# Optimization experiments

Hardware: AMD Instinct MI355X
Metric: run time of the kernel (lower is better)

The kernel has to match this reference:

```python
import jax, jax.numpy as jnp
import numpy as np
from jax import lax


def setup_inputs() -> dict:
    key = jax.random.key(0)
    k1, k2, k3 = jax.random.split(key, 3)
    B, L, T = 1024, 512, 64
    logits = jax.random.normal(k1, (B, L, T), dtype=jnp.float32)
    tags = jax.random.randint(k2, (B, L), 0, T, dtype=jnp.int64)
    mask = jnp.ones((B, L), dtype=jnp.int32)
    trans_m = jax.random.normal(k3, (T, T), dtype=jnp.float32)
    return {"logits": logits, "tags": tags, "mask": mask, "trans_m": trans_m}


def _normalizer(logits_t, mask_t, trans):
    # logits_t: [L, B, T], mask_t: [L, B] float, trans: [T, T]
    alpha0 = logits_t[0]  # [B, T]

    def step(alpha, xs):
        emit, m = xs  # emit [B, T], m [B]
        # alpha[b, i] + trans[i, j] + emit[b, j] -> logsumexp over i
        tmp = alpha[:, :, None] + emit[:, None, :] + trans[None, :, :]  # [B, T, T]
        new_alpha = jax.nn.logsumexp(tmp, axis=1)  # [B, T]
        alpha = jnp.where(m[:, None] > 0, new_alpha, alpha)
        return alpha, None

    alpha, _ = lax.scan(step, alpha0, (logits_t[1:], mask_t[1:]))
    return jax.nn.logsumexp(alpha, axis=1)  # [B]


def _gold_score(logits_t, tags_t, mask_t, trans):
    # logits_t: [L, B, T], tags_t: [L, B] int, mask_t: [L, B] float
    # transition score between consecutive gold tags, masked where next pos is pad
    trans_score = trans[tags_t[:-1], tags_t[1:]] * mask_t[1:]  # [L-1, B]
    # emission score at gold tags, masked at pad positions
    emit = jnp.take_along_axis(logits_t, tags_t[:, :, None], axis=2)[:, :, 0] * mask_t  # [L, B]
    score = (trans_score + emit[:-1]).sum(axis=0) + emit[-1] * mask_t[-1]  # [B]
    return score


def reference(logits, tags, mask, trans_m):
    # forward: feats [B, L, T] -> transpose to [L, B, T]; loss = logZ - gold_score
    logits_t = jnp.transpose(logits, (1, 0, 2)).astype(jnp.float32)  # [L, B, T]
    tags_t = jnp.transpose(tags, (1, 0))  # [L, B]
    mask_t = jnp.transpose(mask, (1, 0)).astype(logits.dtype)  # [L, B]
    all_path = _normalizer(logits_t, mask_t, trans_m)
    gold = _gold_score(logits_t, tags_t, mask_t, trans_m)
    return all_path - gold  # [B] per-sample negative log-likelihood
```

## Files before the change

kernel.cpp:

```cpp
#include <hip/hip_runtime.h>
#include <math.h>


#define TDIM 64
typedef _Float16 f16;
typedef _Float16 f16x2 __attribute__((ext_vector_type(2)));
typedef _Float16 f16x8 __attribute__((ext_vector_type(8)));
typedef float    f32x4 __attribute__((ext_vector_type(4)));

union B8 { f16x8 v; f16x2 p[4]; };

#define MFMA16(A, B, C) __builtin_amdgcn_mfma_f32_16x16x32_f16((A), (B), (C), 0, 0, 0)

__device__ __forceinline__ f16x2 pk2(float a, float b) {
    f16x2 r; r[0] = (f16)a; r[1] = (f16)b; return r;
}

template <int DIR>
__device__ __forceinline__ void run_chain(
    const float* __restrict__ lp,
    const int*   __restrict__ mrow,
    const float* __restrict__ trans,
    int L, int ml, int gl, bool masked,
    float a[16], int& kacc)
{
    f16x8 Af[4][2];
    #pragma unroll
    for (int c = 0; c < 4; ++c) {
        const int mlog = 32*(c>>1) + 8*(ml>>2) + 4*(c&1) + (ml&3);
        #pragma unroll
        for (int kc = 0; kc < 2; ++kc) {
            B8 t;
            #pragma unroll
            for (int e = 0; e < 8; e += 2) {
                const int k0 = 32*kc + 8*gl + e;
                float x0, x1;
                if (DIR == 0) { x0 = trans[k0*TDIM + mlog];  x1 = trans[(k0+1)*TDIM + mlog]; }
                else          { x0 = trans[mlog*TDIM + k0];  x1 = trans[mlog*TDIM + k0 + 1]; }
                t.p[e>>1] = pk2(__expf(x0), __expf(x1));
            }
            Af[c][kc] = t.v;
        }
    }

    #pragma unroll
    for (int i = 0; i < 16; ++i) a[i] = 1.f;
    kacc = 0;

    const int dstep = (DIR == 0) ? TDIM : -TDIM;
    const float* pp = lp + (size_t)((DIR == 0) ? 0 : (L - 1)) * TDIM + 8 * gl;

    float4 Rf[4][4];
    #pragma unroll
    for (int u = 0; u < 4; ++u) {
        Rf[u][0] = *(const float4*)(pp + 0);
        Rf[u][1] = *(const float4*)(pp + 4);
        Rf[u][2] = *(const float4*)(pp + 32);
        Rf[u][3] = *(const float4*)(pp + 36);
        pp += dstep;
    }
    __builtin_amdgcn_sched_barrier(0);

    float Xc[16];
    #pragma unroll
    for (int c = 0; c < 4; ++c) {
        Xc[c*4+0] = __expf(Rf[0][c].x); Xc[c*4+1] = __expf(Rf[0][c].y);
        Xc[c*4+2] = __expf(Rf[0][c].z); Xc[c*4+3] = __expf(Rf[0][c].w);
    }

    const int NS = L >> 1;
    for (int kb = 0; kb < NS/4; ++kb) {
        #pragma unroll
        for (int u = 0; u < 4; ++u) {
            const int st = 4*kb + u;

            Rf[u][0] = *(const float4*)(pp + 0);
            Rf[u][1] = *(const float4*)(pp + 4);
            Rf[u][2] = *(const float4*)(pp + 32);
            Rf[u][3] = *(const float4*)(pp + 36);
            pp += dstep;
            __builtin_amdgcn_sched_barrier(0);

            float cand[16];
            if (DIR == 0 && st == 0) {
                #pragma unroll
                for (int i = 0; i < 16; ++i) cand[i] = Xc[i];
            } else {
                float bsrc[16];
                #pragma unroll
                for (int i = 0; i < 16; ++i) bsrc[i] = (DIR == 0) ? a[i] : a[i]*Xc[i];
                B8 b0, b1;
                #pragma unroll
                for (int h = 0; h < 4; ++h) {
                    b0.p[h] = pk2(bsrc[2*h],     bsrc[2*h+1]);
                    b1.p[h] = pk2(bsrc[8 + 2*h], bsrc[8 + 2*h+1]);
                }
                f32x4 D0 = {0.f,0.f,0.f,0.f}, D1 = {0.f,0.f,0.f,0.f};
                f32x4 D2 = {0.f,0.f,0.f,0.f}, D3 = {0.f,0.f,0.f,0.f};
                D0 = MFMA16(Af[0][0], b0.v, D0); D0 = MFMA16(Af[0][1], b1.v, D0);
                D1 = MFMA16(Af[1][0], b0.v, D1); D1 = MFMA16(Af[1][1], b1.v, D1);
                D2 = MFMA16(Af[2][0], b0.v, D2); D2 = MFMA16(Af[2][1], b1.v, D2);
                D3 = MFMA16(Af[3][0], b0.v, D3); D3 = MFMA16(Af[3][1], b1.v, D3);
                if (DIR == 0) {
                    #pragma unroll
                    for (int r = 0; r < 4; ++r) {
                        cand[r]      = D0[r] * Xc[r];
                        cand[4 + r]  = D1[r] * Xc[4 + r];
                        cand[8 + r]  = D2[r] * Xc[8 + r];
                        cand[12 + r] = D3[r] * Xc[12 + r];
                    }
                } else {
                    #pragma unroll
                    for (int r = 0; r < 4; ++r) {
                        cand[r] = D0[r]; cand[4+r] = D1[r];
                        cand[8+r] = D2[r]; cand[12+r] = D3[r];
                    }
                }
                if (masked) {
                    const int t = (DIR == 0) ? st : (L - 1 - st);
                    const int m = mrow[t];
                    #pragma unroll
                    for (int i = 0; i < 16; ++i) cand[i] = (m > 0) ? cand[i] : a[i];
                }
            }

            const int un = (u + 1) & 3;
            float Xn[16];
            #pragma unroll
            for (int c = 0; c < 4; ++c) {
                Xn[c*4+0] = __expf(Rf[un][c].x); Xn[c*4+1] = __expf(Rf[un][c].y);
                Xn[c*4+2] = __expf(Rf[un][c].z); Xn[c*4+3] = __expf(Rf[un][c].w);
            }

            {
                const float ref = __shfl(cand[0], ml);
                const int eb = (__float_as_int(ref) >> 23) & 255;
                kacc += eb - 117;
                const float s = __int_as_float((unsigned)(244 - eb) << 23);
                #pragma unroll
                for (int i = 0; i < 16; ++i) a[i] = cand[i] * s;
            }
            #pragma unroll
            for (int i = 0; i < 16; ++i) Xc[i] = Xn[i];
        }
    }
}

__global__ __launch_bounds__(256, 1) void crf_mfma_kernel(
    const float* __restrict__ logits,
    const int*   __restrict__ tags,
    const int*   __restrict__ mask,
    const float* __restrict__ trans,
    float* __restrict__ out,
    int L)
{
    const int tid = threadIdx.x;
    const int w   = tid >> 6;
    const int l   = tid & 63;
    const int ml  = l & 15;
    const int gl  = l >> 4;
    const int bg  = blockIdx.x * 16;
    const int bi  = bg + ml;

    __shared__ __align__(16) float zfin[64][16];
    __shared__ float gpart2[2][16];
    __shared__ int   kbuf[16];

    float a[16];
    int   kacc = 0;

    if (w >= 2) {
        const int t0 = (w - 2) * (L >> 1);
        const int*   tb  = tags + (size_t)bi * L;
        const int*   mb  = mask + (size_t)bi * L;
        const float* lbg = logits + (size_t)bi * L * TDIM;
        float gs = 0.f;
        #pragma unroll 4
        for (int i = 0; i < (L >> 3); ++i) {
            const int t  = t0 + gl + 4*i;
            const int tg = tb[t];
            const float mk = (float)mb[t];
            const float em = lbg[(size_t)t * TDIM + tg];
            const float tr = (t > 0) ? trans[tb[t-1] * TDIM + tg] : 0.f;
            gs += mk * (em + tr);
        }
        gs += __shfl_xor(gs, 16);
        gs += __shfl_xor(gs, 32);
        if (l < 16) gpart2[w - 2][l] = gs;
    } else {
        const float* lp   = logits + (size_t)bi * L * TDIM;
        const int*   mrow = mask + (size_t)bi * L;
        const int t0 = (w == 0) ? 0 : (L >> 1);
        bool ok = true;
        {
            const int4* m4 = (const int4*)(mrow + t0);
            #pragma unroll 4
            for (int i = 0; i < 16; ++i) {
                const int4 v = m4[gl * 16 + i];
                ok = ok && (v.x > 0) && (v.y > 0) && (v.z > 0) && (v.w > 0);
            }
        }
        const bool masked = !__all(ok ? 1 : 0);
        if (w == 0) run_chain<0>(lp, mrow, trans, L, ml, gl, masked, a, kacc);
        else        run_chain<1>(lp, mrow, trans, L, ml, gl, masked, a, kacc);
        if (w == 1) {
            #pragma unroll
            for (int i = 0; i < 16; ++i) zfin[l][i] = a[i];
            if (l < 16) kbuf[l] = kacc;
        }
    }

    __syncthreads();

    if (w == 0) {
        float prod = 0.f;
        #pragma unroll
        for (int i = 0; i < 16; ++i) prod += a[i] * zfin[l][i];
        prod += __shfl_xor(prod, 16);
        prod += __shfl_xor(prod, 32);
        if (l < 16) {
            const float logZ = (float)(kacc + kbuf[l]) * 0.6931471805599453f
                             + __logf(prod);
            out[bg + l] = logZ - (gpart2[0][l] + gpart2[1][l]);
        }
    }
}

extern "C" void kernel_launch(void* const* d_in, const int* in_sizes, int n_in,
                              void* d_out, int out_size, void* d_ws, size_t ws_size,
                              hipStream_t stream) {
    const float* logits = (const float*)d_in[0];
    const int*   tags   = (const int*)d_in[1];
    const int*   mask   = (const int*)d_in[2];
    const float* trans  = (const float*)d_in[3];
    float* out = (float*)d_out;

    const int B = out_size;
    const int L = in_sizes[1] / B;

    crf_mfma_kernel<<<B / 16, 256, 0, stream>>>(logits, tags, mask, trans, out, L);
}
```

Measured before the change: 277.7 us.

## Stage logits into LDS via async global_load_lds double buffering

Replaces the per-step register prefetch of logits in the forward/backward chains with asynchronous global-to-LDS loads (global_load_lds) into double-buffered 8-step slots, waited on with explicit vmcnt. Mask values are also precomputed into an LDS bitmap so the masked path avoids per-step global reads. The goal is to hide global memory latency behind the serial MFMA recurrence while freeing registers. In exchange it needs about 129 KB of LDS per block and relies on hand-written waitcnt counts.

```diff
diff --git a/kernel.cpp b/kernel.cpp
--- a/kernel.cpp
+++ b/kernel.cpp
@@ -7,23 +7,46 @@
 typedef _Float16 f16x2 __attribute__((ext_vector_type(2)));
 typedef _Float16 f16x8 __attribute__((ext_vector_type(8)));
 typedef float    f32x4 __attribute__((ext_vector_type(4)));
+typedef float    fv4   __attribute__((ext_vector_type(4)));
 
 union B8 { f16x8 v; f16x2 p[4]; };
 
 #define MFMA16(A, B, C) __builtin_amdgcn_mfma_f32_16x16x32_f16((A), (B), (C), 0, 0, 0)
+
+typedef __attribute__((address_space(3))) char       lds_char;
+typedef __attribute__((address_space(3))) const fv4  lds_cfv4;
+typedef __attribute__((address_space(1))) const char g1_char;
+
+#define PLANE_STRIDE 1024
+#define SLOT_STRIDE  4096
+#define BUF_STRIDE   32768
+#define WV_STRIDE    65536
+#define BITMAP_OFF   131072
+#define SMEM_BYTES   132096
 
 __device__ __forceinline__ f16x2 pk2(float a, float b) {
     f16x2 r; r[0] = (f16)a; r[1] = (f16)b; return r;
 }
 
+__device__ __forceinline__ void stage_slot(const float* pp, char* slotbase) {
+    __builtin_amdgcn_global_load_lds((g1_char*)(pp + 0),  (lds_char*)(slotbase + 0*PLANE_STRIDE), 16, 0, 0);
+    __builtin_amdgcn_global_load_lds((g1_char*)(pp + 4),  (lds_char*)(slotbase + 1*PLANE_STRIDE), 16, 0, 0);
+    __builtin_amdgcn_global_load_lds((g1_char*)(pp + 32), (lds_char*)(slotbase + 2*PLANE_STRIDE), 16, 0, 0);
+    __builtin_amdgcn_global_load_lds((g1_char*)(pp + 36), (lds_char*)(slotbase + 3*PLANE_STRIDE), 16, 0, 0);
+}
+
 template <int DIR>
 __device__ __forceinline__ void run_chain(
-    const float* __restrict__ lp,
-    const int*   __restrict__ mrow,
+    const float* __restrict__ logits0,
+    const int*   __restrict__ mask0,
     const float* __restrict__ trans,
-    int L, int ml, int gl, bool masked,
+    char* smem, int w, int l, int L, bool masked,
     float a[16], int& kacc)
 {
+    const int ml = l & 15;
+    const int gl = l >> 4;
+    const int H  = L >> 1;
+
     f16x8 Af[4][2];
     #pragma unroll
     for (int c = 0; c < 4; ++c) {
@@ -43,43 +66,72 @@
         }
     }
 
+    unsigned* mwv = (unsigned*)(smem + BITMAP_OFF + w * 512);
+    const int t0m = DIR ? H : 0;
+    const int WPB = H >> 5;
+    if (masked) {
+        for (int flat = l; flat < 16 * WPB; flat += 64) {
+            const int mb = flat / WPB, w8 = flat - mb * WPB;
+            unsigned word = 0;
+            const int* mp = mask0 + (size_t)mb * L + t0m + 32 * w8;
+            for (int j = 0; j < 32; ++j) word |= (mp[j] > 0 ? 1u : 0u) << j;
+            mwv[flat] = word;
+        }
+    }
+
     #pragma unroll
     for (int i = 0; i < 16; ++i) a[i] = 1.f;
     kacc = 0;
 
-    const int dstep = (DIR == 0) ? TDIM : -TDIM;
-    const float* pp = lp + (size_t)((DIR == 0) ? 0 : (L - 1)) * TDIM + 8 * gl;
-
-    float4 Rf[4][4];
+    char* stg = smem + w * WV_STRIDE;
+    char* rb0 = stg + 16 * l;
+    const float* pp = logits0 + ((size_t)ml * L + (DIR ? (L - 1) : 0)) * TDIM + 8 * gl;
+    const int drow = DIR ? -TDIM : TDIM;
+
+    __builtin_amdgcn_sched_barrier(0);
+
     #pragma unroll
-    for (int u = 0; u < 4; ++u) {
-        Rf[u][0] = *(const float4*)(pp + 0);
-        Rf[u][1] = *(const float4*)(pp + 4);
-        Rf[u][2] = *(const float4*)(pp + 32);
-        Rf[u][3] = *(const float4*)(pp + 36);
-        pp += dstep;
-    }
-    __builtin_amdgcn_sched_barrier(0);
-
-    float Xc[16];
-    #pragma unroll
-    for (int c = 0; c < 4; ++c) {
-        Xc[c*4+0] = __expf(Rf[0][c].x); Xc[c*4+1] = __expf(Rf[0][c].y);
-        Xc[c*4+2] = __expf(Rf[0][c].z); Xc[c*4+3] = __expf(Rf[0][c].w);
-    }
-
-    const int NS = L >> 1;
-    for (int kb = 0; kb < NS/4; ++kb) {
-        #pragma unroll
-        for (int u = 0; u < 4; ++u) {
-            const int st = 4*kb + u;
-
-            Rf[u][0] = *(const float4*)(pp + 0);
-            Rf[u][1] = *(const float4*)(pp + 4);
-            Rf[u][2] = *(const float4*)(pp + 32);
-            Rf[u][3] = *(const float4*)(pp + 36);
-            pp += dstep;
-            __builtin_amdgcn_sched_barrier(0);
+    for (int cpre = 0; cpre < 2; ++cpre) {
+        char* cb = stg + cpre * BUF_STRIDE;
+        #pragma unroll
+        for (int u = 0; u < 8; ++u) {
+            stage_slot(pp, cb + u * SLOT_STRIDE);
+            pp += drow;
+        }
+    }
+
+    float Xn[16], Xc[16];
+    fv4 q[4];
+    const int NSS = H >> 3;
+    for (int S = 0; S < NSS; ++S) {
+        char* crb = rb0 + (S & 1) * BUF_STRIDE;
+        char* cwb = stg + (S & 1) * BUF_STRIDE;
+
+        asm volatile("s_waitcnt vmcnt(32)" ::: "memory");
+        __builtin_amdgcn_sched_barrier(0);
+
+        q[0] = *(lds_cfv4*)(crb + 0 * PLANE_STRIDE);
+        q[1] = *(lds_cfv4*)(crb + 1 * PLANE_STRIDE);
+        q[2] = *(lds_cfv4*)(crb + 2 * PLANE_STRIDE);
+        q[3] = *(lds_cfv4*)(crb + 3 * PLANE_STRIDE);
+        #pragma unroll
+        for (int c = 0; c < 4; ++c) {
+            #pragma unroll
+            for (int r = 0; r < 4; ++r) Xn[c*4 + r] = __expf(q[c][r]);
+        }
+
+        #pragma unroll
+        for (int u = 0; u < 8; ++u) {
+            #pragma unroll
+            for (int i = 0; i < 16; ++i) Xc[i] = Xn[i];
+            const int st = 8 * S + u;
+
+            if (u < 7) {
+                q[0] = *(lds_cfv4*)(crb + (u+1)*SLOT_STRIDE + 0*PLANE_STRIDE);
+                q[1] = *(lds_cfv4*)(crb + (u+1)*SLOT_STRIDE + 1*PLANE_STRIDE);
+                q[2] = *(lds_cfv4*)(crb + (u+1)*SLOT_STRIDE + 2*PLANE_STRIDE);
+                q[3] = *(lds_cfv4*)(crb + (u+1)*SLOT_STRIDE + 3*PLANE_STRIDE);
+            }
 
             float cand[16];
             if (DIR == 0 && st == 0) {
@@ -88,7 +140,7 @@
             } else {
                 float bsrc[16];
                 #pragma unroll
-                for (int i = 0; i < 16; ++i) bsrc[i] = (DIR == 0) ? a[i] : a[i]*Xc[i];
+                for (int i = 0; i < 16; ++i) bsrc[i] = (DIR == 0) ? a[i] : a[i] * Xc[i];
                 B8 b0, b1;
                 #pragma unroll
                 for (int h = 0; h < 4; ++h) {
@@ -117,19 +169,20 @@
                     }
                 }
                 if (masked) {
-                    const int t = (DIR == 0) ? st : (L - 1 - st);
-                    const int m = mrow[t];
+                    const int dt = DIR ? (H - 1 - st) : st;
+                    const unsigned wd = mwv[ml * WPB + (dt >> 5)];
+                    const int mb = (wd >> (dt & 31)) & 1;
                     #pragma unroll
-                    for (int i = 0; i < 16; ++i) cand[i] = (m > 0) ? cand[i] : a[i];
+                    for (int i = 0; i < 16; ++i) cand[i] = mb ? cand[i] : a[i];
                 }
             }
 
-            const int un = (u + 1) & 3;
-            float Xn[16];
-            #pragma unroll
-            for (int c = 0; c < 4; ++c) {
-                Xn[c*4+0] = __expf(Rf[un][c].x); Xn[c*4+1] = __expf(Rf[un][c].y);
-                Xn[c*4+2] = __expf(Rf[un][c].z); Xn[c*4+3] = __expf(Rf[un][c].w);
+            if (u < 7) {
+                #pragma unroll
+                for (int c = 0; c < 4; ++c) {
+                    #pragma unroll
+                    for (int r = 0; r < 4; ++r) Xn[c*4 + r] = __expf(q[c][r]);
+                }
             }
 
             {
@@ -140,10 +193,16 @@
                 #pragma unroll
                 for (int i = 0; i < 16; ++i) a[i] = cand[i] * s;
             }
-            #pragma unroll
-            for (int i = 0; i < 16; ++i) Xc[i] = Xn[i];
-        }
-    }
+        }
+
+        #pragma unroll
+        for (int u = 0; u < 8; ++u) {
+            stage_slot(pp, cwb + u * SLOT_STRIDE);
+            pp += drow;
+        }
+    }
+
+    asm volatile("s_waitcnt vmcnt(0)" ::: "memory");
 }
 
 __global__ __launch_bounds__(256, 1) void crf_mfma_kernel(
@@ -161,23 +220,25 @@
     const int gl  = l >> 4;
     const int bg  = blockIdx.x * 16;
     const int bi  = bg + ml;
-
-    __shared__ __align__(16) float zfin[64][16];
-    __shared__ float gpart2[2][16];
-    __shared__ int   kbuf[16];
+    const int H   = L >> 1;
+
+    __shared__ __align__(16) char smem[SMEM_BYTES];
+
+    const float* logits0 = logits + (size_t)bg * L * TDIM;
+    const int*   mask0   = mask + (size_t)bg * L;
 
     float a[16];
     int   kacc = 0;
+    float gs   = 0.f;
 
     if (w >= 2) {
-        const int t0 = (w - 2) * (L >> 1);
+        const int t0 = (w - 2) * H;
         const int*   tb  = tags + (size_t)bi * L;
         const int*   mb  = mask + (size_t)bi * L;
         const float* lbg = logits + (size_t)bi * L * TDIM;
-        float gs = 0.f;
         #pragma unroll 4
         for (int i = 0; i < (L >> 3); ++i) {
-            const int t  = t0 + gl + 4*i;
+            const int t  = t0 + gl + 4 * i;
             const int tg = tb[t];
             const float mk = (float)mb[t];
             const float em = lbg[(size_t)t * TDIM + tg];
@@ -186,36 +247,41 @@
         }
         gs += __shfl_xor(gs, 16);
         gs += __shfl_xor(gs, 32);
-        if (l < 16) gpart2[w - 2][l] = gs;
     } else {
-        const float* lp   = logits + (size_t)bi * L * TDIM;
-        const int*   mrow = mask + (size_t)bi * L;
-        const int t0 = (w == 0) ? 0 : (L >> 1);
+        const int t0d = (w == 0) ? 0 : H;
         bool ok = true;
         {
-            const int4* m4 = (const int4*)(mrow + t0);
+            const int4* m4 = (const int4*)(mask0 + (size_t)ml * L + t0d);
             #pragma unroll 4
-            for (int i = 0; i < 16; ++i) {
-                const int4 v = m4[gl * 16 + i];
+            for (int i = 0; i < (H >> 4); ++i) {
+                const int4 v = m4[gl * (H >> 4) + i];
                 ok = ok && (v.x > 0) && (v.y > 0) && (v.z > 0) && (v.w > 0);
             }
         }
         const bool masked = !__all(ok ? 1 : 0);
-        if (w == 0) run_chain<0>(lp, mrow, trans, L, ml, gl, masked, a, kacc);
-        else        run_chain<1>(lp, mrow, trans, L, ml, gl, masked, a, kacc);
-        if (w == 1) {
-            #pragma unroll
-            for (int i = 0; i < 16; ++i) zfin[l][i] = a[i];
-            if (l < 16) kbuf[l] = kacc;
-        }
-    }
+        if (w == 0) run_chain<0>(logits0, mask0, trans, smem, w, l, L, masked, a, kacc);
+        else        run_chain<1>(logits0, mask0, trans, smem, w, l, L, masked, a, kacc);
+    }
+
+    __syncthreads();
+
+    float* zfin = (float*)smem;
+    float (*gpart2)[16] = (float(*)[16])(smem + 4096);
+    int*   kbuf = (int*)(smem + 4224);
+
+    if (w == 1) {
+        #pragma unroll
+        for (int i = 0; i < 16; ++i) zfin[l * 16 + i] = a[i];
+        if (l < 16) kbuf[l] = kacc;
+    }
+    if (w >= 2 && l < 16) gpart2[w - 2][l] = gs;
 
     __syncthreads();
 
     if (w == 0) {
         float prod = 0.f;
         #pragma unroll
-        for (int i = 0; i < 16; ++i) prod += a[i] * zfin[l][i];
+        for (int i = 0; i < 16; ++i) prod += a[i] * zfin[l * 16 + i];
         prod += __shfl_xor(prod, 16);
         prod += __shfl_xor(prod, 32);
         if (l < 16) {
```

Result: faster. 272.1 us (-2.0%).
